# Kernel tuning notes

Measured on AMD Instinct MI355X. Metric: run time of the kernel, lower is better.

Reference implementation:

```python
import jax, jax.numpy as jnp
import numpy as np

N_NODES = 50000


def _sage_max(x, src, dst, W_l, b_l, W_r):
    # gather neighbor (source) features, scatter-max to destination nodes
    msgs = x[src]                                   # [E, F]
    agg = jax.ops.segment_max(msgs, dst, num_segments=N_NODES)  # [N, F], -inf for empty
    agg = jnp.where(jnp.isneginf(agg), 0.0, agg)    # PyG fills isolated nodes with 0
    return agg @ W_l + b_l + x @ W_r                # lin_l(aggr) + lin_r(x)


def setup_inputs() -> dict:
    key = jax.random.key(0)
    ks = jax.random.split(key, 9)
    F_IN, H, OUT, E, EL = 128, 256, 32, 800000, 200000
    x = jax.random.normal(ks[0], (N_NODES, F_IN), dtype=jnp.float32)
    edge_index = jax.random.randint(ks[1], (2, E), 0, N_NODES, dtype=jnp.int64)
    edge_label_index = jax.random.randint(ks[2], (2, EL), 0, N_NODES, dtype=jnp.int64)
    s1 = 1.0 / np.sqrt(F_IN)
    s2 = 1.0 / np.sqrt(H)
    W1_l = jax.random.normal(ks[3], (F_IN, H), dtype=jnp.float32) * s1
    b1 = jnp.zeros((H,), dtype=jnp.float32)
    W1_r = jax.random.normal(ks[4], (F_IN, H), dtype=jnp.float32) * s1
    W2_l = jax.random.normal(ks[5], (H, OUT), dtype=jnp.float32) * s2
    b2 = jnp.zeros((OUT,), dtype=jnp.float32)
    W2_r = jax.random.normal(ks[6], (H, OUT), dtype=jnp.float32) * s2
    return {"x": x, "edge_index": edge_index, "edge_label_index": edge_label_index,
            "W1_l": W1_l, "b1": b1, "W1_r": W1_r,
            "W2_l": W2_l, "b2": b2, "W2_r": W2_r}


def reference(x, edge_index, edge_label_index, W1_l, b1, W1_r, W2_l, b2, W2_r):
    src, dst = edge_index[0], edge_index[1]
    # encode (eval mode: dropout is identity)
    h = jax.nn.relu(_sage_max(x, src, dst, W1_l, b1, W1_r))
    z = _sage_max(h, src, dst, W2_l, b2, W2_r)       # [N, 32]
    # decode: dot product between endpoint embeddings
    s = z[edge_label_index[0]]
    d = z[edge_label_index[1]]
    return jnp.sum(s * d, axis=-1)                   # [E_label]
```

## Files before the change

### kernel.cpp

```cpp
#include <hip/hip_runtime.h>
#include <hip/hip_bf16.h>
#include <math.h>

#define N_NODES 50000
#define NBKT 196
#define BSH 8
#define TILE2 4096
#define CAP 64
#define P2CAP 5888
#define SCAN_FLAG 0x40000000

typedef __attribute__((ext_vector_type(8))) short short8;
typedef __attribute__((ext_vector_type(4))) float f32x4;

static __device__ __forceinline__ float b2f(unsigned int u16) {
    union { unsigned int i; float f; } c; c.i = u16 << 16; return c.f;
}
static __device__ __forceinline__ unsigned int fbits(float f) {
    union { float f; unsigned int i; } c; c.f = f; return c.i;
}
static __device__ __forceinline__ unsigned short f2b_rne(float f) {
    unsigned int u = fbits(f);
    u += 0x7fff + ((u >> 16) & 1);
    return (unsigned short)(u >> 16);
}

static __device__ __forceinline__ unsigned char quant8(float v) {
    int q = (int)(v * 15.9375f + 0.5f);
    return (unsigned char)min(q, 255);
}
static __device__ __forceinline__ float dequant8(int b) {
    return (float)b * 0.0627451f;
}


__global__ __launch_bounds__(256) void k_prepbin(
        const float* __restrict__ x, unsigned short* __restrict__ xb,
        const float* __restrict__ W1l, const float* __restrict__ W1r, unsigned short* __restrict__ wt1,
        const float* __restrict__ W2l, const float* __restrict__ W2r, unsigned short* __restrict__ wt2,
        float* __restrict__ zb,
        const int* __restrict__ src, const int* __restrict__ dst, int E,
        uint2* __restrict__ tmp, int* __restrict__ cnts, int ntile) {
    __shared__ int cnt[256], sstart[256], lcur[256];
    __shared__ uint2 stage[TILE2];
    const int CX = (N_NODES * 128 / 4) / 256;
    const int CW = CX + 320;
    const int CZ = CW + 1563;
    int b = blockIdx.x, t = threadIdx.x;
    if (b < CX) {
        int i = b * 256 + t;
        float4 v = *(const float4*)(x + (size_t)i * 4);
        ushort4 o;
        o.x = f2b_rne(v.x); o.y = f2b_rne(v.y); o.z = f2b_rne(v.z); o.w = f2b_rne(v.w);
        *(ushort4*)(xb + (size_t)i * 4) = o;
    } else if (b < CX + 256) {
        int i = (b - CX) * 256 + t;
        int n = i >> 8, k = i & 255;
        float v = (k < 128) ? W1l[(size_t)k * 256 + n] : W1r[(size_t)(k - 128) * 256 + n];
        wt1[(size_t)n * 256 + k] = f2b_rne(v);
    } else if (b < CW) {
        int i = (b - CX - 256) * 256 + t;
        int n = i >> 9, k = i & 511;
        float v = (k < 256) ? W2l[(size_t)k * 32 + n] : W2r[(size_t)(k - 256) * 32 + n];
        wt2[(size_t)n * 512 + k] = f2b_rne(v);
    } else if (b < CZ) {
        int i = (b - CW) * 256 + t;
        if (i < 400000) ((float4*)zb)[i] = (float4){0.f, 0.f, 0.f, 0.f};
    } else {
        int tb = b - CZ;
        int e0 = tb * TILE2;
        int tilecnt = min(TILE2, E - e0);
        if (tilecnt <= 0) return;
        cnt[t] = 0;
        __syncthreads();
        if (tilecnt == TILE2) {
            for (int i = 4 * t; i < TILE2; i += 1024) {
                int4 d = *(const int4*)(dst + e0 + i);
                atomicAdd(&cnt[d.x >> BSH], 1);
                atomicAdd(&cnt[d.y >> BSH], 1);
                atomicAdd(&cnt[d.z >> BSH], 1);
                atomicAdd(&cnt[d.w >> BSH], 1);
            }
        } else {
            for (int i = t; i < tilecnt; i += 256)
                atomicAdd(&cnt[dst[e0 + i] >> BSH], 1);
        }
        __syncthreads();
        int cv = cnt[t];
        sstart[t] = cv;
        __syncthreads();
        for (int off = 1; off < 256; off <<= 1) {
            int add = (t >= off) ? sstart[t - off] : 0;
            __syncthreads();
            sstart[t] += add;
            __syncthreads();
        }
        int mystart = sstart[t] - cv;
        __syncthreads();
        sstart[t] = mystart;
        lcur[t] = mystart;
        __syncthreads();
        if (tilecnt == TILE2) {
            for (int i = 4 * t; i < TILE2; i += 1024) {
                int4 d = *(const int4*)(dst + e0 + i);
                int4 s = *(const int4*)(src + e0 + i);
                int q0 = atomicAdd(&lcur[d.x >> BSH], 1); stage[q0] = (uint2){(unsigned)s.x, (unsigned)d.x};
                int q1 = atomicAdd(&lcur[d.y >> BSH], 1); stage[q1] = (uint2){(unsigned)s.y, (unsigned)d.y};
                int q2 = atomicAdd(&lcur[d.z >> BSH], 1); stage[q2] = (uint2){(unsigned)s.z, (unsigned)d.z};
                int q3 = atomicAdd(&lcur[d.w >> BSH], 1); stage[q3] = (uint2){(unsigned)s.w, (unsigned)d.w};
            }
        } else {
            for (int i = t; i < tilecnt; i += 256) {
                int d = dst[e0 + i];
                int s = src[e0 + i];
                int q = atomicAdd(&lcur[d >> BSH], 1);
                uint2 p; p.x = (unsigned)s; p.y = (unsigned)d;
                stage[q] = p;
            }
        }
        __syncthreads();
        if (t < NBKT) cnts[(size_t)t * ntile + tb] = cnt[t];
        for (int i = t; i < tilecnt; i += 256) {
            uint2 p = stage[i];
            int bk = (int)(p.y >> BSH);
            tmp[((size_t)bk * ntile + tb) * CAP + (i - sstart[bk])] = p;
        }
    }
}


__global__ __launch_bounds__(256) void k_bin2(const uint2* __restrict__ tmp,
        const int* __restrict__ cnts, int* __restrict__ pub,
        int* __restrict__ rowptr, int* __restrict__ esrc, int N, int E, int ntile) {
    __shared__ int sc[256], toff[260], nodecnt[256], lcur[256];
    __shared__ int stage[P2CAP];
    __shared__ int shsum[4];
    int k = blockIdx.x, t = threadIdx.x;

    int c = (t < ntile) ? cnts[(size_t)k * ntile + t] : 0;
    sc[t] = c;
    __syncthreads();
    for (int off = 1; off < 256; off <<= 1) {
        int add = (t >= off) ? sc[t - off] : 0;
        __syncthreads();
        sc[t] += add;
        __syncthreads();
    }
    if (t < ntile) toff[t] = sc[t] - c;
    if (t == 255) toff[ntile] = sc[255];
    __syncthreads();
    int total = toff[ntile];

    if (t == 255) atomicExch(&pub[k], SCAN_FLAG | total);
    int v = 0;
    if (t < k) {
        int val;
        do { val = atomicOr(&pub[t], 0); } while (!(val & SCAN_FLAG) || (val & 0x80000000));
        v = val & (SCAN_FLAG - 1);
    }
#pragma unroll
    for (int off = 32; off >= 1; off >>= 1) v += __shfl_xor(v, off);
    if ((t & 63) == 0) shsum[t >> 6] = v;
    nodecnt[t] = 0;
    __syncthreads();
    int base = shsum[0] + shsum[1] + shsum[2] + shsum[3];

    for (int i = t; i < total; i += 256) {
        int lo = 0, hi = ntile;
        while (hi - lo > 1) { int mid = (lo + hi) >> 1; if (toff[mid] <= i) lo = mid; else hi = mid; }
        uint2 p = tmp[((size_t)k * ntile + lo) * CAP + (i - toff[lo])];
        atomicAdd(&nodecnt[(int)p.y & 255], 1);
    }
    __syncthreads();

    int nc = nodecnt[t];
    sc[t] = nc;
    __syncthreads();
    for (int off = 1; off < 256; off <<= 1) {
        int add = (t >= off) ? sc[t - off] : 0;
        __syncthreads();
        sc[t] += add;
        __syncthreads();
    }
    int ex = sc[t] - nc;
    int node = (k << BSH) + t;
    if (node < N) rowptr[node] = base + ex;
    if (node == N) rowptr[N] = E;
    lcur[t] = ex;
    __syncthreads();

    if (total <= P2CAP) {
        for (int i = t; i < total; i += 256) {
            int lo = 0, hi = ntile;
            while (hi - lo > 1) { int mid = (lo + hi) >> 1; if (toff[mid] <= i) lo = mid; else hi = mid; }
            uint2 p = tmp[((size_t)k * ntile + lo) * CAP + (i - toff[lo])];
            int q = atomicAdd(&lcur[(int)p.y & 255], 1);
            stage[q] = (int)p.x;
        }
        __syncthreads();
        for (int i = t; i < total; i += 256)
            esrc[base + i] = stage[i];
    } else {
        for (int i = t; i < total; i += 256) {
            int lo = 0, hi = ntile;
            while (hi - lo > 1) { int mid = (lo + hi) >> 1; if (toff[mid] <= i) lo = mid; else hi = mid; }
            uint2 p = tmp[((size_t)k * ntile + lo) * CAP + (i - toff[lo])];
            int q = atomicAdd(&lcur[(int)p.y & 255], 1);
            esrc[base + q] = (int)p.x;
        }
    }
}


__global__ __launch_bounds__(256) void k_seg_max1(const unsigned short* __restrict__ feat,
        const int* __restrict__ rowptr, const int* __restrict__ esrc,
        unsigned short* __restrict__ out) {
    int w = threadIdx.x >> 6, t = threadIdx.x & 63;
    int n = blockIdx.x * 4 + w;
    int lane16 = t & 15, sub = t >> 4;
    int beg = rowptr[n], end = rowptr[n + 1];
    float m[8];
#pragma unroll
    for (int k = 0; k < 8; ++k) m[k] = -INFINITY;
    for (int base = beg; base < end; base += 64) {
        int cnt = min(64, end - base);
        int vidx = (base + t < end) ? __builtin_nontemporal_load(&esrc[base + t]) : 0;
        for (int j = 0; j < cnt; j += 16) {
            uint4 v[4];
#pragma unroll
            for (int u = 0; u < 4; ++u) {
                int e = min(j + 4 * u + sub, cnt - 1);
                int s = __shfl(vidx, e);
                v[u] = *(const uint4*)(feat + (size_t)s * 128 + lane16 * 8);
            }
#pragma unroll
            for (int u = 0; u < 4; ++u) {
                m[0] = fmaxf(m[0], b2f(v[u].x & 0xffff));
                m[1] = fmaxf(m[1], b2f(v[u].x >> 16));
                m[2] = fmaxf(m[2], b2f(v[u].y & 0xffff));
                m[3] = fmaxf(m[3], b2f(v[u].y >> 16));
                m[4] = fmaxf(m[4], b2f(v[u].z & 0xffff));
                m[5] = fmaxf(m[5], b2f(v[u].z >> 16));
                m[6] = fmaxf(m[6], b2f(v[u].w & 0xffff));
                m[7] = fmaxf(m[7], b2f(v[u].w >> 16));
            }
        }
    }
#pragma unroll
    for (int k = 0; k < 8; ++k) {
        m[k] = fmaxf(m[k], __shfl_xor(m[k], 16));
        m[k] = fmaxf(m[k], __shfl_xor(m[k], 32));
        if (beg == end) m[k] = 0.f;
    }
    if (sub == 0) {
        uint4 p;
        p.x = (fbits(m[0]) >> 16) | (fbits(m[1]) & 0xffff0000u);
        p.y = (fbits(m[2]) >> 16) | (fbits(m[3]) & 0xffff0000u);
        p.z = (fbits(m[4]) >> 16) | (fbits(m[5]) & 0xffff0000u);
        p.w = (fbits(m[6]) >> 16) | (fbits(m[7]) & 0xffff0000u);
        *(uint4*)(out + (size_t)n * 128 + lane16 * 8) = p;
    }
}


__global__ __launch_bounds__(256) void k_seg_max2(const unsigned char* __restrict__ feat8,
        const int* __restrict__ rowptr, const int* __restrict__ esrc,
        unsigned char* __restrict__ out8) {
    int w = threadIdx.x >> 6, t = threadIdx.x & 63;
    int n = blockIdx.x * 4 + w;
    int lane16 = t & 15, sub = t >> 4;
    int beg = rowptr[n], end = rowptr[n + 1];
    int m[16];
#pragma unroll
    for (int k = 0; k < 16; ++k) m[k] = 0;
    for (int base = beg; base < end; base += 64) {
        int cnt = min(64, end - base);
        int vidx = (base + t < end) ? __builtin_nontemporal_load(&esrc[base + t]) : 0;
        for (int j = 0; j < cnt; j += 32) {
            uint4 v[8];
#pragma unroll
            for (int u = 0; u < 8; ++u) {
                int e = min(j + 4 * u + sub, cnt - 1);
                int s = __shfl(vidx, e);
                v[u] = *(const uint4*)(feat8 + (size_t)s * 256 + lane16 * 16);
            }
#pragma unroll
            for (int u = 0; u < 8; ++u) {
                m[0]  = max(m[0],  (int)(v[u].x & 0xFF));
                m[1]  = max(m[1],  (int)((v[u].x >> 8) & 0xFF));
                m[2]  = max(m[2],  (int)((v[u].x >> 16) & 0xFF));
                m[3]  = max(m[3],  (int)(v[u].x >> 24));
                m[4]  = max(m[4],  (int)(v[u].y & 0xFF));
                m[5]  = max(m[5],  (int)((v[u].y >> 8) & 0xFF));
                m[6]  = max(m[6],  (int)((v[u].y >> 16) & 0xFF));
                m[7]  = max(m[7],  (int)(v[u].y >> 24));
                m[8]  = max(m[8],  (int)(v[u].z & 0xFF));
                m[9]  = max(m[9],  (int)((v[u].z >> 8) & 0xFF));
                m[10] = max(m[10], (int)((v[u].z >> 16) & 0xFF));
                m[11] = max(m[11], (int)(v[u].z >> 24));
                m[12] = max(m[12], (int)(v[u].w & 0xFF));
                m[13] = max(m[13], (int)((v[u].w >> 8) & 0xFF));
                m[14] = max(m[14], (int)((v[u].w >> 16) & 0xFF));
                m[15] = max(m[15], (int)(v[u].w >> 24));
            }
        }
    }
#pragma unroll
    for (int k = 0; k < 16; ++k) {
        m[k] = max(m[k], __shfl_xor(m[k], 16));
        m[k] = max(m[k], __shfl_xor(m[k], 32));
    }
    if (sub == 0) {
        uint4 p;
        p.x = m[0]  | (m[1]  << 8) | (m[2]  << 16) | (m[3]  << 24);
        p.y = m[4]  | (m[5]  << 8) | (m[6]  << 16) | (m[7]  << 24);
        p.z = m[8]  | (m[9]  << 8) | (m[10] << 16) | (m[11] << 24);
        p.w = m[12] | (m[13] << 8) | (m[14] << 16) | (m[15] << 24);
        *(uint4*)(out8 + (size_t)n * 256 + lane16 * 16) = p;
    }
}


__global__ __launch_bounds__(256) void k_lin1_mfma(
        const unsigned short* __restrict__ A0, const unsigned short* __restrict__ A1,
        const unsigned short* __restrict__ WT, const float* __restrict__ bias,
        const unsigned short* __restrict__ WT2, float* __restrict__ zpart,
        unsigned char* __restrict__ H8, int M) {
    __shared__ short sh[16640];
    __shared__ short Bs2[32 * 136];
    short* As = sh;
    short* Bs = sh + 5120;
    short* Hs = sh;

    int tid = threadIdx.x;
    int m0 = blockIdx.y * 128, n0 = blockIdx.x * 128;
    int L = tid & 63, wv = tid >> 6;
    int wr = wv >> 1, wc = wv & 1;
    int lane16 = L & 15, q = L >> 4;

    {
        int n = tid >> 3, kc = (tid & 7) * 16;
        *(float4*)&Bs2[n * 136 + kc] =
            *(const float4*)(WT2 + (size_t)n * 512 + 256 + n0 + kc);
        *(float4*)&Bs2[n * 136 + kc + 8] =
            *(const float4*)(WT2 + (size_t)n * 512 + 256 + n0 + kc + 8);
    }

    f32x4 acc[4][4];
#pragma unroll
    for (int i = 0; i < 4; ++i)
#pragma unroll
        for (int j = 0; j < 4; ++j) acc[i][j] = (f32x4){0.f, 0.f, 0.f, 0.f};

    for (int k0 = 0; k0 < 256; k0 += 32) {
        const unsigned short* Abase = (k0 < 128) ? A0 : A1;
        int kc = k0 & 127;
#pragma unroll
        for (int s = tid; s < 512; s += 256) {
            int m = s >> 2, sg = s & 3;
            int row = m0 + m;
            float4 v = {0.f, 0.f, 0.f, 0.f};
            if (row < M) v = *(const float4*)(Abase + (size_t)row * 128 + kc + sg * 8);
            *(float4*)&As[m * 40 + sg * 8] = v;
        }
#pragma unroll
        for (int s = tid; s < 512; s += 256) {
            int n = s >> 2, sg = s & 3;
            *(float4*)&Bs[n * 40 + sg * 8] =
                *(const float4*)(WT + (size_t)(n0 + n) * 256 + k0 + sg * 8);
        }
        __syncthreads();

        short8 a[4], b[4];
#pragma unroll
        for (int i = 0; i < 4; ++i)
            a[i] = *(const short8*)&As[(wr * 64 + i * 16 + lane16) * 40 + q * 8];
#pragma unroll
        for (int j = 0; j < 4; ++j)
            b[j] = *(const short8*)&Bs[(wc * 64 + j * 16 + lane16) * 40 + q * 8];
#pragma unroll
        for (int i = 0; i < 4; ++i)
#pragma unroll
            for (int j = 0; j < 4; ++j)
                acc[i][j] = __builtin_amdgcn_mfma_f32_16x16x32_bf16(a[i], b[j], acc[i][j], 0, 0, 0);
        __syncthreads();
    }

#pragma unroll
    for (int i = 0; i < 4; ++i) {
#pragma unroll
        for (int r = 0; r < 4; ++r) {
            int lrow = wr * 64 + i * 16 + q * 4 + r;
            int row = m0 + lrow;
#pragma unroll
            for (int j = 0; j < 4; ++j) {
                int lcol = wc * 64 + j * 16 + lane16;
                int col = n0 + lcol;
                float v = fmaxf(acc[i][j][r] + bias[col], 0.f);
                unsigned short hb16 = f2b_rne(v);
                Hs[lrow * 130 + lcol] = (short)hb16;
                if (row < M) H8[(size_t)row * 256 + col] = quant8(v);
            }
        }
    }
    __syncthreads();

    f32x4 acc2[2][2];
#pragma unroll
    for (int i = 0; i < 2; ++i)
#pragma unroll
        for (int j = 0; j < 2; ++j) acc2[i][j] = (f32x4){0.f, 0.f, 0.f, 0.f};
#pragma unroll
    for (int kk = 0; kk < 4; ++kk) {
        short8 a2[2], b2[2];
#pragma unroll
        for (int i = 0; i < 2; ++i)
            a2[i] = *(const short8*)&Hs[(wv * 32 + i * 16 + lane16) * 130 + kk * 32 + q * 8];
#pragma unroll
        for (int j = 0; j < 2; ++j)
            b2[j] = *(const short8*)&Bs2[(j * 16 + lane16) * 136 + kk * 32 + q * 8];
#pragma unroll
        for (int i = 0; i < 2; ++i)
#pragma unroll
            for (int j = 0; j < 2; ++j)
                acc2[i][j] = __builtin_amdgcn_mfma_f32_16x16x32_bf16(a2[i], b2[j], acc2[i][j], 0, 0, 0);
    }
#pragma unroll
    for (int i = 0; i < 2; ++i) {
#pragma unroll
        for (int r = 0; r < 4; ++r) {
            int row = m0 + wv * 32 + i * 16 + q * 4 + r;
            if (row >= M) continue;
#pragma unroll
            for (int j = 0; j < 2; ++j) {
                int col = j * 16 + lane16;
                atomicAdd(&zpart[(size_t)row * 32 + col], acc2[i][j][r]);
            }
        }
    }
}


__global__ __launch_bounds__(256) void k_lin2_mfma(
        const unsigned char* __restrict__ A8,
        const unsigned short* __restrict__ WT, const float* __restrict__ bias,
        float* __restrict__ Z, int M) {
    __shared__ short As[128 * 40];
    __shared__ short Bs[32 * 40];

    int tid = threadIdx.x;
    int m0 = blockIdx.x * 128;
    int L = tid & 63, wv = tid >> 6;
    int lane16 = L & 15, q = L >> 4;

    f32x4 acc[2][2];
#pragma unroll
    for (int i = 0; i < 2; ++i)
#pragma unroll
        for (int j = 0; j < 2; ++j) acc[i][j] = (f32x4){0.f, 0.f, 0.f, 0.f};

    for (int k0 = 0; k0 < 256; k0 += 32) {
#pragma unroll
        for (int s = tid; s < 512; s += 256) {
            int m = s >> 2, sg = s & 3;
            int row = m0 + m;
            uint2 v8 = {0u, 0u};
            if (row < M) v8 = *(const uint2*)(A8 + (size_t)row * 256 + k0 + sg * 8);
            unsigned short e[8];
#pragma unroll
            for (int bi = 0; bi < 4; ++bi)
                e[bi] = f2b_rne((float)((v8.x >> (8 * bi)) & 255u) * 0.0627451f);
#pragma unroll
            for (int bi = 0; bi < 4; ++bi)
                e[4 + bi] = f2b_rne((float)((v8.y >> (8 * bi)) & 255u) * 0.0627451f);
            uint4 p;
            p.x = e[0] | ((unsigned)e[1] << 16);
            p.y = e[2] | ((unsigned)e[3] << 16);
            p.z = e[4] | ((unsigned)e[5] << 16);
            p.w = e[6] | ((unsigned)e[7] << 16);
            *(uint4*)&As[m * 40 + sg * 8] = p;
        }
        if (tid < 128) {
            int n = tid >> 2, sg = tid & 3;
            *(float4*)&Bs[n * 40 + sg * 8] =
                *(const float4*)(WT + (size_t)n * 512 + k0 + sg * 8);
        }
        __syncthreads();

        short8 a[2], b[2];
#pragma unroll
        for (int i = 0; i < 2; ++i)
            a[i] = *(const short8*)&As[(wv * 32 + i * 16 + lane16) * 40 + q * 8];
#pragma unroll
        for (int j = 0; j < 2; ++j)
            b[j] = *(const short8*)&Bs[(j * 16 + lane16) * 40 + q * 8];
#pragma unroll
        for (int i = 0; i < 2; ++i)
#pragma unroll
            for (int j = 0; j < 2; ++j)
                acc[i][j] = __builtin_amdgcn_mfma_f32_16x16x32_bf16(a[i], b[j], acc[i][j], 0, 0, 0);
        __syncthreads();
    }

#pragma unroll
    for (int i = 0; i < 2; ++i) {
#pragma unroll
        for (int r = 0; r < 4; ++r) {
            int row = m0 + wv * 32 + i * 16 + q * 4 + r;
            if (row >= M) continue;
#pragma unroll
            for (int j = 0; j < 2; ++j) {
                int col = j * 16 + lane16;
                float zp = Z[(size_t)row * 32 + col];
                Z[(size_t)row * 32 + col] = acc[i][j][r] + bias[col] + zp;
            }
        }
    }
}


__global__ void k_decode(const float* __restrict__ z, const int* __restrict__ eli,
                         int EL, float* __restrict__ out) {
    int tid = blockIdx.x * blockDim.x + threadIdx.x;
    int e = tid >> 3, lane = tid & 7;
    if (e >= EL) return;
    int s = eli[e], d = eli[EL + e];
    float4 a = *((const float4*)(z + (size_t)s * 32) + lane);
    float4 b = *((const float4*)(z + (size_t)d * 32) + lane);
    float dot = a.x * b.x + a.y * b.y + a.z * b.z + a.w * b.w;
    dot += __shfl_xor(dot, 1);
    dot += __shfl_xor(dot, 2);
    dot += __shfl_xor(dot, 4);
    if (lane == 0) out[e] = dot;
}


extern "C" void kernel_launch(void* const* d_in, const int* in_sizes, int n_in,
                              void* d_out, int out_size, void* d_ws, size_t ws_size,
                              hipStream_t stream) {
    const float* x   = (const float*)d_in[0];
    const int*   ei  = (const int*)d_in[1];
    const int*   eli = (const int*)d_in[2];
    const float* W1l = (const float*)d_in[3];
    const float* b1  = (const float*)d_in[4];
    const float* W1r = (const float*)d_in[5];
    const float* W2l = (const float*)d_in[6];
    const float* b2  = (const float*)d_in[7];
    const float* W2r = (const float*)d_in[8];
    float* out = (float*)d_out;

    int N  = N_NODES;
    int E  = in_sizes[1] / 2;
    int EL = in_sizes[2] / 2;
    const int* src = ei;
    const int* dst = ei + E;

    char* ws = (char*)d_ws;
    size_t off = 0;
    auto alloc = [&](size_t bytes) -> void* {
        void* p = ws + off;
        off += (bytes + 255) & ~(size_t)255;
        return p;
    };
    unsigned short* xb   = (unsigned short*)alloc((size_t)N * 128 * 2);
    unsigned short* aggb = (unsigned short*)alloc((size_t)N * 256 * 2);
    unsigned char*  h8   = (unsigned char*)alloc((size_t)N * 256);
    float* zbuf          = (float*)alloc((size_t)N * 32 * 4);
    unsigned short* wt1  = (unsigned short*)alloc(256 * 256 * 2);
    unsigned short* wt2  = (unsigned short*)alloc(32 * 512 * 2);
    int* rowptr   = (int*)alloc((size_t)(N + 1) * 4);
    int ntile     = (E + TILE2 - 1) / TILE2;
    int* cnts     = (int*)alloc((size_t)NBKT * ntile * 4);
    int* pub      = (int*)alloc(256 * 4);
    int* esrc     = (int*)alloc((size_t)E * 4);
    uint2* tmpp   = (uint2*)aggb;
    unsigned char* agg8 = (unsigned char*)aggb;

    const int tb = 256;
    const int CZ = 6250 + 320 + 1563;

    k_prepbin<<<CZ + ntile, tb, 0, stream>>>(x, xb, W1l, W1r, wt1, W2l, W2r, wt2, zbuf,
                                             src, dst, E, tmpp, cnts, ntile);
    k_bin2<<<NBKT, tb, 0, stream>>>(tmpp, cnts, pub, rowptr, esrc, N, E, ntile);

    k_seg_max1<<<(N + 3) / 4, tb, 0, stream>>>(xb, rowptr, esrc, aggb);
    dim3 g1(2, (N + 127) / 128);
    k_lin1_mfma<<<g1, tb, 0, stream>>>(aggb, xb, wt1, b1, wt2, zbuf, h8, N);

    k_seg_max2<<<(N + 3) / 4, tb, 0, stream>>>(h8, rowptr, esrc, agg8);
    k_lin2_mfma<<<(N + 127) / 128, tb, 0, stream>>>(agg8, wt2, b2, zbuf, N);

    k_decode<<<(EL * 8 + 255) / 256, tb, 0, stream>>>(zbuf, eli, EL, out);
}
```

Baseline: 253.0 us.

## Load MFMA operands directly from global memory, drop LDS staging in linear kernels

Both the lin1 and lin2 GEMM kernels now load their A and B fragments straight from global memory into registers in MFMA layout, instead of staging tiles through shared memory with two barriers per k-step. The second-layer weight tile in lin1 is also read directly from global rather than preloaded into LDS, and the hidden-tile buffer is re-padded to a 136 stride. This removes LDS traffic and synchronisation, but gives up tile reuse across waves. Each wave re-fetches A and B rows from L2/global with 16-byte strided accesses that may coalesce less well.

```diff
diff --git a/kernel.cpp b/kernel.cpp
--- a/kernel.cpp
+++ b/kernel.cpp
@@ -29,8 +29,16 @@
     int q = (int)(v * 15.9375f + 0.5f);
     return (unsigned char)min(q, 255);
 }
-static __device__ __forceinline__ float dequant8(int b) {
-    return (float)b * 0.0627451f;
+
+static __device__ __forceinline__ short8 dq8(uint2 v8) {
+    short8 r;
+#pragma unroll
+    for (int bi = 0; bi < 4; ++bi)
+        r[bi] = (short)f2b_rne((float)((v8.x >> (8 * bi)) & 255u) * 0.0627451f);
+#pragma unroll
+    for (int bi = 0; bi < 4; ++bi)
+        r[4 + bi] = (short)f2b_rne((float)((v8.y >> (8 * bi)) & 255u) * 0.0627451f);
+    return r;
 }
 
 
@@ -326,11 +334,7 @@
         const unsigned short* __restrict__ WT, const float* __restrict__ bias,
         const unsigned short* __restrict__ WT2, float* __restrict__ zpart,
         unsigned char* __restrict__ H8, int M) {
-    __shared__ short sh[16640];
-    __shared__ short Bs2[32 * 136];
-    short* As = sh;
-    short* Bs = sh + 5120;
-    short* Hs = sh;
+    __shared__ short Hs[128 * 136];
 
     int tid = threadIdx.x;
     int m0 = blockIdx.y * 128, n0 = blockIdx.x * 128;
@@ -338,52 +342,35 @@
     int wr = wv >> 1, wc = wv & 1;
     int lane16 = L & 15, q = L >> 4;
 
-    {
-        int n = tid >> 3, kc = (tid & 7) * 16;
-        *(float4*)&Bs2[n * 136 + kc] =
-            *(const float4*)(WT2 + (size_t)n * 512 + 256 + n0 + kc);
-        *(float4*)&Bs2[n * 136 + kc + 8] =
-            *(const float4*)(WT2 + (size_t)n * 512 + 256 + n0 + kc + 8);
-    }
-
     f32x4 acc[4][4];
 #pragma unroll
     for (int i = 0; i < 4; ++i)
 #pragma unroll
         for (int j = 0; j < 4; ++j) acc[i][j] = (f32x4){0.f, 0.f, 0.f, 0.f};
 
+    const short8 zero8 = (short8){0, 0, 0, 0, 0, 0, 0, 0};
+    int arow[4], brow[4];
+#pragma unroll
+    for (int i = 0; i < 4; ++i) arow[i] = m0 + wr * 64 + i * 16 + lane16;
+#pragma unroll
+    for (int j = 0; j < 4; ++j) brow[j] = n0 + wc * 64 + j * 16 + lane16;
+
+#pragma unroll 1
     for (int k0 = 0; k0 < 256; k0 += 32) {
         const unsigned short* Abase = (k0 < 128) ? A0 : A1;
-        int kc = k0 & 127;
-#pragma unroll
-        for (int s = tid; s < 512; s += 256) {
-            int m = s >> 2, sg = s & 3;
-            int row = m0 + m;
-            float4 v = {0.f, 0.f, 0.f, 0.f};
-            if (row < M) v = *(const float4*)(Abase + (size_t)row * 128 + kc + sg * 8);
-            *(float4*)&As[m * 40 + sg * 8] = v;
-        }
-#pragma unroll
-        for (int s = tid; s < 512; s += 256) {
-            int n = s >> 2, sg = s & 3;
-            *(float4*)&Bs[n * 40 + sg * 8] =
-                *(const float4*)(WT + (size_t)(n0 + n) * 256 + k0 + sg * 8);
-        }
-        __syncthreads();
-
+        int kc = (k0 & 127) + q * 8;
         short8 a[4], b[4];
 #pragma unroll
         for (int i = 0; i < 4; ++i)
-            a[i] = *(const short8*)&As[(wr * 64 + i * 16 + lane16) * 40 + q * 8];
+            a[i] = (arow[i] < M) ? *(const short8*)(Abase + (size_t)arow[i] * 128 + kc) : zero8;
 #pragma unroll
         for (int j = 0; j < 4; ++j)
-            b[j] = *(const short8*)&Bs[(wc * 64 + j * 16 + lane16) * 40 + q * 8];
+            b[j] = *(const short8*)(WT + (size_t)brow[j] * 256 + k0 + q * 8);
 #pragma unroll
         for (int i = 0; i < 4; ++i)
 #pragma unroll
             for (int j = 0; j < 4; ++j)
                 acc[i][j] = __builtin_amdgcn_mfma_f32_16x16x32_bf16(a[i], b[j], acc[i][j], 0, 0, 0);
-        __syncthreads();
     }
 
 #pragma unroll
@@ -397,8 +384,7 @@
                 int lcol = wc * 64 + j * 16 + lane16;
                 int col = n0 + lcol;
                 float v = fmaxf(acc[i][j][r] + bias[col], 0.f);
-                unsigned short hb16 = f2b_rne(v);
-                Hs[lrow * 130 + lcol] = (short)hb16;
+                Hs[lrow * 136 + lcol] = (short)f2b_rne(v);
                 if (row < M) H8[(size_t)row * 256 + col] = quant8(v);
             }
         }
@@ -415,10 +401,10 @@
         short8 a2[2], b2[2];
 #pragma unroll
         for (int i = 0; i < 2; ++i)
-            a2[i] = *(const short8*)&Hs[(wv * 32 + i * 16 + lane16) * 130 + kk * 32 + q * 8];
+            a2[i] = *(const short8*)&Hs[(wv * 32 + i * 16 + lane16) * 136 + kk * 32 + q * 8];
 #pragma unroll
         for (int j = 0; j < 2; ++j)
-            b2[j] = *(const short8*)&Bs2[(j * 16 + lane16) * 136 + kk * 32 + q * 8];
+            b2[j] = *(const short8*)(WT2 + (size_t)(j * 16 + lane16) * 512 + 256 + n0 + kk * 32 + q * 8);
 #pragma unroll
         for (int i = 0; i < 2; ++i)
 #pragma unroll
@@ -445,9 +431,6 @@
         const unsigned char* __restrict__ A8,
         const unsigned short* __restrict__ WT, const float* __restrict__ bias,
         float* __restrict__ Z, int M) {
-    __shared__ short As[128 * 40];
-    __shared__ short Bs[32 * 40];
-
     int tid = threadIdx.x;
     int m0 = blockIdx.x * 128;
     int L = tid & 63, wv = tid >> 6;
@@ -459,47 +442,27 @@
 #pragma unroll
         for (int j = 0; j < 2; ++j) acc[i][j] = (f32x4){0.f, 0.f, 0.f, 0.f};
 
+    int arow[2];
+#pragma unroll
+    for (int i = 0; i < 2; ++i) arow[i] = m0 + wv * 32 + i * 16 + lane16;
+
+#pragma unroll 1
     for (int k0 = 0; k0 < 256; k0 += 32) {
-#pragma unroll
-        for (int s = tid; s < 512; s += 256) {
-            int m = s >> 2, sg = s & 3;
-            int row = m0 + m;
-            uint2 v8 = {0u, 0u};
-            if (row < M) v8 = *(const uint2*)(A8 + (size_t)row * 256 + k0 + sg * 8);
-            unsigned short e[8];
-#pragma unroll
-            for (int bi = 0; bi < 4; ++bi)
-                e[bi] = f2b_rne((float)((v8.x >> (8 * bi)) & 255u) * 0.0627451f);
-#pragma unroll
-            for (int bi = 0; bi < 4; ++bi)
-                e[4 + bi] = f2b_rne((float)((v8.y >> (8 * bi)) & 255u) * 0.0627451f);
-            uint4 p;
-            p.x = e[0] | ((unsigned)e[1] << 16);
-            p.y = e[2] | ((unsigned)e[3] << 16);
-            p.z = e[4] | ((unsigned)e[5] << 16);
-            p.w = e[6] | ((unsigned)e[7] << 16);
-            *(uint4*)&As[m * 40 + sg * 8] = p;
-        }
-        if (tid < 128) {
-            int n = tid >> 2, sg = tid & 3;
-            *(float4*)&Bs[n * 40 + sg * 8] =
-                *(const float4*)(WT + (size_t)n * 512 + k0 + sg * 8);
-        }
-        __syncthreads();
-
         short8 a[2], b[2];
 #pragma unroll
-        for (int i = 0; i < 2; ++i)
-            a[i] = *(const short8*)&As[(wv * 32 + i * 16 + lane16) * 40 + q * 8];
+        for (int i = 0; i < 2; ++i) {
+            uint2 v8 = (arow[i] < M) ? *(const uint2*)(A8 + (size_t)arow[i] * 256 + k0 + q * 8)
+                                     : (uint2){0u, 0u};
+            a[i] = dq8(v8);
+        }
 #pragma unroll
         for (int j = 0; j < 2; ++j)
-            b[j] = *(const short8*)&Bs[(j * 16 + lane16) * 40 + q * 8];
+            b[j] = *(const short8*)(WT + (size_t)(j * 16 + lane16) * 512 + k0 + q * 8);
 #pragma unroll
         for (int i = 0; i < 2; ++i)
 #pragma unroll
             for (int j = 0; j < 2; ++j)
                 acc[i][j] = __builtin_amdgcn_mfma_f32_16x16x32_bf16(a[i], b[j], acc[i][j], 0, 0, 0);
-        __syncthreads();
     }
 
 #pragma unroll
```

Result: no change. 256.5 us (+1.3%).
